# Kernel optimization log

Hardware: AMD Instinct MI355X
Metric: run time of the kernel (lower is better)

## Reference

```python
import jax, jax.numpy as jnp
import numpy as np

EPS = 1.0  # Shapelet eps
STRIDE = 1


def _shapelet(x, w, pcm):
    """x: (b,c,t), w: (n,c,l), pcm: (c,m). Returns ((b, n*c) probs, (b, n*c) dists)."""
    n, c, l = w.shape
    t = x.shape[-1]
    m = (t - l) // STRIDE + 1
    # unfold: gather overlapping windows -> (b, c, m, l)
    idx = jnp.arange(m)[:, None] * STRIDE + jnp.arange(l)[None, :]
    win = x[:, :, idx]                                   # (b, c, m, l)
    xw = jnp.transpose(win, (0, 2, 1, 3))[:, :, None]    # (b, m, 1, c, l)
    d = jnp.mean(jnp.abs(xw - w), axis=-1)               # (b, m, n, c)
    d = d * pcm.T[None, :, None, :]                      # penalty (1, m, 1, c)
    p = jnp.exp(-jnp.square(EPS * d))                    # (b, m, n, c)
    hard = jax.nn.one_hot(jnp.argmax(p, axis=1), m, axis=1, dtype=p.dtype)  # (b,m,n,c)
    soft = jax.nn.softmax(p, axis=1)
    onehot_max = hard + soft - jax.lax.stop_gradient(soft)  # straight-through
    max_p = jnp.sum(onehot_max * p, axis=1)              # (b, n, c)
    d_min = jnp.min(d, axis=1)                           # (b, n, c)
    b = x.shape[0]
    return max_p.reshape(b, -1), d_min.reshape(b, -1)


def _diversity(w):
    """w: (n,c,l) -> scalar. torch PairwiseDistance(p=2, eps=1e-6) adds eps to diff."""
    sh = jnp.transpose(w, (1, 0, 2))                     # (c, n, l)
    diff = sh[:, None, :, :] - sh[:, :, None, :] + 1e-6
    dist = jnp.sqrt(jnp.sum(jnp.square(diff), axis=-1))  # (c, n, n)
    nsh = sh.shape[1]
    mask = 1.0 - jnp.eye(nsh, dtype=w.dtype)
    return jnp.mean(jnp.exp(-dist) * mask[None])


def setup_inputs() -> dict:
    key = jax.random.key(0)
    ks = jax.random.split(key, 6)
    b, c, t, ncls = 32, 8, 512, 10
    sls = [52, 103, 154, 256]
    ms = [t - l + 1 for l in sls]
    inp = {"x": jax.random.normal(ks[0], (b, c, t), dtype=jnp.float32)}
    for i, (l, m) in enumerate(zip(sls, ms)):
        inp[f"w{i}"] = jax.random.normal(ks[1 + i], (5, c, l), dtype=jnp.float32)
        inp[f"pcm{i}"] = jnp.ones((c, m), dtype=jnp.float32)
    inp["W_out"] = jax.random.normal(ks[5], (ncls, 160), dtype=jnp.float32) * 0.05
    return inp


def reference(x, w0, w1, w2, w3, pcm0, pcm1, pcm2, pcm3, W_out):
    # instance norm over time (torch std is unbiased, ddof=1)
    mu = jnp.mean(x, axis=-1, keepdims=True)
    sd = jnp.std(x, axis=-1, keepdims=True, ddof=1)
    xn = (x - mu) / (sd + 1e-8)

    ws = (w0, w1, w2, w3)
    pcms = (pcm0, pcm1, pcm2, pcm3)
    probs, dists = [], []
    for w, pcm in zip(ws, pcms):
        p, d = _shapelet(xn, w, pcm)
        probs.append(p)
        dists.append(d)
    shapelet_probs = jnp.concatenate(probs, axis=-1)   # (b, 160)
    shapelet_dists = jnp.concatenate(dists, axis=-1)   # (b, 160)

    # dropout is identity in eval mode
    out = shapelet_probs @ W_out.T                     # (b, num_classes)

    loss_reg = jnp.mean(jnp.abs(W_out))
    loss_div = sum(_diversity(w) for w in ws)
    loss = (0.1 * loss_reg + 0.1 * loss_div).reshape(1)
    return out, shapelet_dists, shapelet_probs, loss
```

## Files before the change

kernel.cpp:

```cpp
#include <hip/hip_runtime.h>
#include <math.h>

#define B 32
#define C 8
#define T 512
#define NSH 5
#define NCLS 10
#define NFEAT 160

#define OUT_OFF    0
#define DIST_OFF   (B * NCLS)
#define PROB_OFF   (DIST_OFF + B * NFEAT)
#define LOSS_OFF   (PROB_OFF + B * NFEAT)

#define MUINV_OFF 648

__global__ __launch_bounds__(256) void prep_kernel(
    const float* __restrict__ x,
    const float* __restrict__ w0, const float* __restrict__ w1,
    const float* __restrict__ w2, const float* __restrict__ w3,
    const float* __restrict__ Wout,
    float* __restrict__ wsf)
{
    const int blk  = blockIdx.x;
    const int wv   = __builtin_amdgcn_readfirstlane(threadIdx.x >> 6);
    const int lane = threadIdx.x & 63;

    if (blk < 64) {
        const int bc = blk * 4 + wv;
        const float* xr = x + bc * T;
        const float4 u0 = *(const float4*)(xr + lane * 4);
        const float4 u1 = *(const float4*)(xr + 256 + lane * 4);
        float s = u0.x + u0.y + u0.z + u0.w + u1.x + u1.y + u1.z + u1.w;
        #pragma unroll
        for (int off = 32; off; off >>= 1) s += __shfl_down(s, off);
        const float mu = __shfl(s, 0) * (1.0f / T);
        float sq = (u0.x-mu)*(u0.x-mu) + (u0.y-mu)*(u0.y-mu) + (u0.z-mu)*(u0.z-mu) + (u0.w-mu)*(u0.w-mu)
                 + (u1.x-mu)*(u1.x-mu) + (u1.y-mu)*(u1.y-mu) + (u1.z-mu)*(u1.z-mu) + (u1.w-mu)*(u1.w-mu);
        #pragma unroll
        for (int off = 32; off; off >>= 1) sq += __shfl_down(sq, off);
        if (lane == 0) {
            const float var = sq * (1.0f / (T - 1));
            const float ns  = 1.0f / (sqrtf(var) + 1e-8f);
            wsf[MUINV_OFF + 2*bc]     = ns;
            wsf[MUINV_OFF + 2*bc + 1] = -mu * ns;
        }
    } else if (blk < 224) {
        const int task = (blk - 64) * 4 + wv;
        const int g  = task / 160;
        const int r  = task - g * 160;
        const int c  = r / 20;
        const int pr = r - c * 20;
        const int i  = pr >> 2;
        const int j0 = pr & 3;
        const int j  = j0 + (j0 >= i ? 1 : 0);
        const float* wptrs[4] = { w0, w1, w2, w3 };
        const int    Ls[4]    = { 52, 103, 154, 256 };
        const int L = Ls[g];
        const float* wi = wptrs[g] + (i * C + c) * L;
        const float* wj = wptrs[g] + (j * C + c) * L;
        float ss = 0.0f;
        for (int t2 = lane; t2 < L; t2 += 64) {
            const float df = wj[t2] - wi[t2] + 1e-6f;
            ss += df * df;
        }
        #pragma unroll
        for (int off = 32; off; off >>= 1) ss += __shfl_down(ss, off);
        if (lane == 0) wsf[task] = expf(-sqrtf(ss));
    } else {
        float rg = 0.0f;
        #pragma unroll
        for (int k2 = 0; k2 < 7; ++k2) {
            const int e = lane + k2 * 64;
            if (e < 400) rg += fabsf(Wout[wv * 400 + e]);
        }
        #pragma unroll
        for (int off = 32; off; off >>= 1) rg += __shfl_down(rg, off);
        if (lane == 0) wsf[640 + wv] = rg;
    }
}

template<int L, int M, int GOFF, int MPL, int CW>
__device__ __forceinline__ void shapelet_task(
    const float* __restrict__ xrow,
    const float* __restrict__ wrow,
    const float* __restrict__ pmrow,
    const float* __restrict__ minv2,
    float* __restrict__ out, int b, int c, int n)
{
    const int lane  = threadIdx.x & 63;
    const int sbase = lane * MPL;
    const int sb = (sbase < M) ? sbase : 0;

    const float ns = minv2[0];
    const float nb = minv2[1];

    float U[16];
    float acc[MPL];
    #pragma unroll
    for (int k = 0; k < MPL; ++k) acc[k] = 0.0f;

    auto LOADCHUNK = [&](int addr) -> float4 {
        int a = addr; if (a > T - 4) a = T - 4;
        if constexpr (CW == 12) {
            return *(const float4*)(xrow + a);
        } else {
            const float2 lo = *(const float2*)(xrow + a);
            const float2 hi = *(const float2*)(xrow + a + 2);
            return float4{lo.x, lo.y, hi.x, hi.y};
        }
    };

    if constexpr (CW == 12) {
        #pragma unroll
        for (int q = 0; q < 3; ++q) {
            const float4 v = *(const float4*)(xrow + sb + q * 4);
            U[q*4+0] = fmaf(v.x, ns, nb); U[q*4+1] = fmaf(v.y, ns, nb);
            U[q*4+2] = fmaf(v.z, ns, nb); U[q*4+3] = fmaf(v.w, ns, nb);
        }
    } else {
        #pragma unroll
        for (int q = 0; q < 5; ++q) {
            const float2 v = *(const float2*)(xrow + sb + q * 2);
            U[q*2+0] = fmaf(v.x, ns, nb); U[q*2+1] = fmaf(v.y, ns, nb);
        }
    }
    float4 pv0 = LOADCHUNK(sb + CW);
    float4 pv1 = LOADCHUNK(sb + CW + 4);

    int j = 0;

#define PHASE(BB, PV)                                                      \
    {                                                                      \
        U[(BB + CW + 0) & 15] = fmaf(PV.x, ns, nb);                        \
        U[(BB + CW + 1) & 15] = fmaf(PV.y, ns, nb);                        \
        U[(BB + CW + 2) & 15] = fmaf(PV.z, ns, nb);                        \
        U[(BB + CW + 3) & 15] = fmaf(PV.w, ns, nb);                        \
        PV = LOADCHUNK(sb + j + CW + 8);                                   \
        _Pragma("unroll")                                                  \
        for (int jj = 0; jj < 4; ++jj) {                                   \
            const float wj = wrow[j + jj];                                 \
            _Pragma("unroll")                                              \
            for (int k = 0; k < MPL; ++k)                                  \
                acc[k] += fabsf(U[(BB + jj + k) & 15] - wj);               \
        }                                                                  \
        j += 4;                                                            \
    }

    constexpr int NP    = L / 4;
    constexpr int NLOOP = NP / 4;
    constexpr int NTAIL = NP % 4;
    for (int it = 0; it < NLOOP; ++it) {
        PHASE(0,  pv0)
        PHASE(4,  pv1)
        PHASE(8,  pv0)
        PHASE(12, pv1)
    }
    if constexpr (NTAIL >= 1) PHASE(0, pv0)
    if constexpr (NTAIL >= 2) PHASE(4, pv1)
    if constexpr (NTAIL >= 3) PHASE(8, pv0)
#undef PHASE

    if constexpr ((L & 3) != 0) {
        constexpr int TB = (4 * NP) & 15;
        #pragma unroll
        for (int jt = 0; jt < (L & 3); ++jt) {
            const float wj = wrow[4 * NP + jt];
            #pragma unroll
            for (int k = 0; k < MPL; ++k)
                acc[k] += fabsf(U[(TB + jt + k) & 15] - wj);
        }
    }

    constexpr float invL = 1.0f / (float)L;
    float mind = INFINITY, mind2 = INFINITY;
    #pragma unroll
    for (int k = 0; k < MPL; ++k) {
        const int m = sbase + k;
        if (m < M) {
            const float d = acc[k] * invL * pmrow[m];
            mind  = fminf(mind, d);
            mind2 = fminf(mind2, d * d);
        }
    }
    #pragma unroll
    for (int off = 32; off; off >>= 1) {
        mind  = fminf(mind,  __shfl_down(mind,  off));
        mind2 = fminf(mind2, __shfl_down(mind2, off));
    }
    if (lane == 0) {
        const int col = GOFF + n * C + c;
        out[DIST_OFF + b * NFEAT + col] = mind;
        out[PROB_OFF + b * NFEAT + col] = expf(-mind2);
    }
}

__global__ __launch_bounds__(256) void shapelet_kernel(
    const float* __restrict__ x,
    const float* __restrict__ w0, const float* __restrict__ w1,
    const float* __restrict__ w2, const float* __restrict__ w3,
    const float* __restrict__ p0, const float* __restrict__ p1,
    const float* __restrict__ p2, const float* __restrict__ p3,
    float* __restrict__ out, const float* __restrict__ wsf)
{
    const int blk = blockIdx.x;
    const int wv  = __builtin_amdgcn_readfirstlane(threadIdx.x >> 6);

    int gsel, base;
    if      (blk < 320) { gsel = 3; base = 0;   }
    else if (blk < 640) { gsel = 2; base = 320; }
    else if (blk < 960) { gsel = 1; base = 640; }
    else                { gsel = 0; base = 960; }

    const int lt = (blk - base) * 4 + wv;
    const int bc = lt / 5;
    const int n  = lt - bc * 5;
    const int c  = bc & 7;
    const int b  = bc >> 3;
    const float* xr = x + bc * T;
    const float* mi = wsf + MUINV_OFF + 2 * bc;

    switch (gsel) {
        case 3:  shapelet_task<256, 257, 120, 6, 10>(xr, w3 + (n*C+c)*256, p3 + c*257, mi, out, b, c, n); break;
        case 2:  shapelet_task<154, 359,  80, 6, 10>(xr, w2 + (n*C+c)*154, p2 + c*359, mi, out, b, c, n); break;
        case 1:  shapelet_task<103, 410,  40, 8, 12>(xr, w1 + (n*C+c)*103, p1 + c*410, mi, out, b, c, n); break;
        default: shapelet_task< 52, 461,   0, 8, 12>(xr, w0 + (n*C+c)*52,  p0 + c*461, mi, out, b, c, n); break;
    }
}

__global__ __launch_bounds__(64) void head_kernel(
    const float* __restrict__ Wout,
    const float* __restrict__ wsf,
    float* __restrict__ out)
{
    const int blk  = blockIdx.x;
    const int lane = threadIdx.x;
    if (blk < B * NCLS) {
        const int b = blk / NCLS, k = blk - b * NCLS;
        const float* pr = out + PROB_OFF + b * NFEAT;
        const float* wr = Wout + k * NFEAT;
        float acc = 0.0f;
        #pragma unroll
        for (int r = 0; r < 3; ++r) {
            const int f = lane + r * 64;
            if (f < NFEAT) acc += pr[f] * wr[f];
        }
        #pragma unroll
        for (int off = 32; off; off >>= 1) acc += __shfl_down(acc, off);
        if (lane == 0) out[OUT_OFF + blk] = acc;
    } else {
        float dv = 0.0f, rg = 0.0f;
        #pragma unroll
        for (int r = 0; r < 10; ++r) {
            const int i = lane + r * 64;
            if (i < 640) dv += wsf[i];
        }
        if (lane < 4) rg = wsf[640 + lane];
        #pragma unroll
        for (int off = 32; off; off >>= 1) {
            dv += __shfl_down(dv, off);
            rg += __shfl_down(rg, off);
        }
        if (lane == 0)
            out[LOSS_OFF] = 0.1f * (rg * (1.0f / 1600.0f)) + 0.1f * (dv * (1.0f / 200.0f));
    }
}

extern "C" void kernel_launch(void* const* d_in, const int* in_sizes, int n_in,
                              void* d_out, int out_size, void* d_ws, size_t ws_size,
                              hipStream_t stream) {
    const float* x    = (const float*)d_in[0];
    const float* w0   = (const float*)d_in[1];
    const float* pcm0 = (const float*)d_in[2];
    const float* w1   = (const float*)d_in[3];
    const float* pcm1 = (const float*)d_in[4];
    const float* w2   = (const float*)d_in[5];
    const float* pcm2 = (const float*)d_in[6];
    const float* w3   = (const float*)d_in[7];
    const float* pcm3 = (const float*)d_in[8];
    const float* Wout = (const float*)d_in[9];
    float* out = (float*)d_out;
    float* wsf = (float*)d_ws;

    prep_kernel<<<225, 256, 0, stream>>>(x, w0, w1, w2, w3, Wout, wsf);
    shapelet_kernel<<<1280, 256, 0, stream>>>(
        x, w0, w1, w2, w3, pcm0, pcm1, pcm2, pcm3, out, wsf);
    head_kernel<<<B * NCLS + 1, 64, 0, stream>>>(Wout, wsf, out);
}
```

Before: 107.1 us.

## Prefetch shapelet weights into registers and deepen x chunk prefetch

Result: slower. 115.5 us (+7.8%).

```diff
diff --git a/kernel.cpp b/kernel.cpp
--- a/kernel.cpp
+++ b/kernel.cpp
@@ -80,7 +80,7 @@
     }
 }
 
-template<int L, int M, int GOFF, int MPL, int CW>
+template<int L, int M, int GOFF, int MPL, int CW, int ALIGN>
 __device__ __forceinline__ void shapelet_task(
     const float* __restrict__ xrow,
     const float* __restrict__ wrow,
@@ -101,45 +101,58 @@
     for (int k = 0; k < MPL; ++k) acc[k] = 0.0f;
 
     auto LOADCHUNK = [&](int addr) -> float4 {
-        int a = addr; if (a > T - 4) a = T - 4;
-        if constexpr (CW == 12) {
+        int a = addr > (T - 4) ? (T - 4) : addr;
+        if constexpr (ALIGN == 4) {
             return *(const float4*)(xrow + a);
-        } else {
+        } else if constexpr (ALIGN == 2) {
             const float2 lo = *(const float2*)(xrow + a);
             const float2 hi = *(const float2*)(xrow + a + 2);
             return float4{lo.x, lo.y, hi.x, hi.y};
+        } else {
+            return float4{xrow[a], xrow[a+1], xrow[a+2], xrow[a+3]};
         }
     };
 
-    if constexpr (CW == 12) {
-        #pragma unroll
-        for (int q = 0; q < 3; ++q) {
+    if constexpr (ALIGN == 4) {
+        #pragma unroll
+        for (int q = 0; q < CW / 4; ++q) {
             const float4 v = *(const float4*)(xrow + sb + q * 4);
             U[q*4+0] = fmaf(v.x, ns, nb); U[q*4+1] = fmaf(v.y, ns, nb);
             U[q*4+2] = fmaf(v.z, ns, nb); U[q*4+3] = fmaf(v.w, ns, nb);
         }
-    } else {
-        #pragma unroll
-        for (int q = 0; q < 5; ++q) {
+    } else if constexpr (ALIGN == 2) {
+        #pragma unroll
+        for (int q = 0; q < CW / 2; ++q) {
             const float2 v = *(const float2*)(xrow + sb + q * 2);
             U[q*2+0] = fmaf(v.x, ns, nb); U[q*2+1] = fmaf(v.y, ns, nb);
         }
-    }
+    } else {
+        #pragma unroll
+        for (int q = 0; q < CW; ++q)
+            U[q] = fmaf(xrow[sb + q], ns, nb);
+    }
+
     float4 pv0 = LOADCHUNK(sb + CW);
     float4 pv1 = LOADCHUNK(sb + CW + 4);
+    float4 pv2 = LOADCHUNK(sb + CW + 8);
+    float4 pv3 = LOADCHUNK(sb + CW + 12);
+
+    float wc[16];
+    #pragma unroll
+    for (int q = 0; q < 16; ++q) wc[q] = wrow[q];
 
     int j = 0;
 
-#define PHASE(BB, PV)                                                      \
+#define PHASE(BB, PV, WB)                                                  \
     {                                                                      \
         U[(BB + CW + 0) & 15] = fmaf(PV.x, ns, nb);                        \
         U[(BB + CW + 1) & 15] = fmaf(PV.y, ns, nb);                        \
         U[(BB + CW + 2) & 15] = fmaf(PV.z, ns, nb);                        \
         U[(BB + CW + 3) & 15] = fmaf(PV.w, ns, nb);                        \
-        PV = LOADCHUNK(sb + j + CW + 8);                                   \
+        PV = LOADCHUNK(sb + j + CW + 16);                                  \
         _Pragma("unroll")                                                  \
         for (int jj = 0; jj < 4; ++jj) {                                   \
-            const float wj = wrow[j + jj];                                 \
+            const float wj = wc[WB + jj];                                  \
             _Pragma("unroll")                                              \
             for (int k = 0; k < MPL; ++k)                                  \
                 acc[k] += fabsf(U[(BB + jj + k) & 15] - wj);               \
@@ -150,22 +163,32 @@
     constexpr int NP    = L / 4;
     constexpr int NLOOP = NP / 4;
     constexpr int NTAIL = NP % 4;
+
     for (int it = 0; it < NLOOP; ++it) {
-        PHASE(0,  pv0)
-        PHASE(4,  pv1)
-        PHASE(8,  pv0)
-        PHASE(12, pv1)
-    }
-    if constexpr (NTAIL >= 1) PHASE(0, pv0)
-    if constexpr (NTAIL >= 2) PHASE(4, pv1)
-    if constexpr (NTAIL >= 3) PHASE(8, pv0)
+        float nw[16];
+        #pragma unroll
+        for (int q = 0; q < 16; ++q) {
+            int idx = j + 16 + q;
+            idx = (idx < L) ? idx : (L - 1);
+            nw[q] = wrow[idx];
+        }
+        PHASE(0,  pv0, 0)
+        PHASE(4,  pv1, 4)
+        PHASE(8,  pv2, 8)
+        PHASE(12, pv3, 12)
+        #pragma unroll
+        for (int q = 0; q < 16; ++q) wc[q] = nw[q];
+    }
+    if constexpr (NTAIL >= 1) PHASE(0, pv0, 0)
+    if constexpr (NTAIL >= 2) PHASE(4, pv1, 4)
+    if constexpr (NTAIL >= 3) PHASE(8, pv2, 8)
 #undef PHASE
 
     if constexpr ((L & 3) != 0) {
         constexpr int TB = (4 * NP) & 15;
         #pragma unroll
         for (int jt = 0; jt < (L & 3); ++jt) {
-            const float wj = wrow[4 * NP + jt];
+            const float wj = wc[NTAIL * 4 + jt];
             #pragma unroll
             for (int k = 0; k < MPL; ++k)
                 acc[k] += fabsf(U[(TB + jt + k) & 15] - wj);
@@ -221,10 +244,10 @@
     const float* mi = wsf + MUINV_OFF + 2 * bc;
 
     switch (gsel) {
-        case 3:  shapelet_task<256, 257, 120, 6, 10>(xr, w3 + (n*C+c)*256, p3 + c*257, mi, out, b, c, n); break;
-        case 2:  shapelet_task<154, 359,  80, 6, 10>(xr, w2 + (n*C+c)*154, p2 + c*359, mi, out, b, c, n); break;
-        case 1:  shapelet_task<103, 410,  40, 8, 12>(xr, w1 + (n*C+c)*103, p1 + c*410, mi, out, b, c, n); break;
-        default: shapelet_task< 52, 461,   0, 8, 12>(xr, w0 + (n*C+c)*52,  p0 + c*461, mi, out, b, c, n); break;
+        case 3:  shapelet_task<256, 257, 120, 5,  8, 1>(xr, w3 + (n*C+c)*256, p3 + c*257, mi, out, b, c, n); break;
+        case 2:  shapelet_task<154, 359,  80, 6, 10, 2>(xr, w2 + (n*C+c)*154, p2 + c*359, mi, out, b, c, n); break;
+        case 1:  shapelet_task<103, 410,  40, 7, 12, 1>(xr, w1 + (n*C+c)*103, p1 + c*410, mi, out, b, c, n); break;
+        default: shapelet_task< 52, 461,   0, 8, 12, 4>(xr, w0 + (n*C+c)*52,  p0 + c*461, mi, out, b, c, n); break;
     }
 }
 
```
